# Kernel tuning notes

Measured on AMD Instinct MI355X. Metric: run time of the kernel, lower is better.

Reference implementation:

```python
import jax, jax.numpy as jnp
import numpy as np

N_NODES = 100_000
N_EDGES = 3_200_000
NR = 10_000
NRHO = 10_000
CUTOFF = 6.0
RHO_MAX = 60.0


def natural_cubic_coeffs(x, y):
    """Natural cubic spline coefficients. x:[K], y:[K,C] -> a,b,c,d each [K-1,C]."""
    K, C = y.shape
    h = np.diff(x)
    rhs = 6.0 * ((y[2:] - y[1:-1]) / h[1:, None] - (y[1:-1] - y[:-2]) / h[:-1, None])
    n = K - 2
    diag = 2.0 * (h[:-1] + h[1:])
    off = h[1:-1]
    # Thomas algorithm for the tridiagonal system (natural BC: M[0]=M[K-1]=0)
    cp = np.zeros(n)
    dp = np.zeros((n, C))
    cp[0] = off[0] / diag[0] if n > 1 else 0.0
    dp[0] = rhs[0] / diag[0]
    for i in range(1, n):
        denom = diag[i] - off[i - 1] * cp[i - 1]
        if i < n - 1:
            cp[i] = off[i] / denom
        dp[i] = (rhs[i] - off[i - 1] * dp[i - 1]) / denom
    M = np.zeros((K, C))
    M[n] = dp[n - 1]
    for i in range(n - 2, -1, -1):
        M[i + 1] = dp[i] - cp[i] * M[i + 2]
    a = y[:-1]
    b = (y[1:] - y[:-1]) / h[:, None] - h[:, None] * (2.0 * M[:-1] + M[1:]) / 6.0
    c = M[:-1] / 2.0
    d = (M[1:] - M[:-1]) / (6.0 * h[:, None])
    f32 = lambda z: jnp.asarray(z, dtype=jnp.float32)
    return f32(a), f32(b), f32(c), f32(d)


def spline_eval(x, knots, a, b, c, d):
    """Piecewise cubic eval. x:[M], knots:[K], coeffs:[K-1,C] -> [M,C]."""
    idx = jnp.clip(jnp.searchsorted(knots, x, side='right') - 1, 0, knots.shape[0] - 2)
    s = (x - knots[idx])[:, None]  # offset within segment
    return a[idx] + s * (b[idx] + s * (c[idx] + s * d[idx]))


def setup_inputs() -> dict:
    key = jax.random.key(0)
    k1, k2, k3 = jax.random.split(key, 3)
    # edge displacement vectors; norms ~ chi(3)*1.2, well within cutoff
    r = jax.random.normal(k1, (N_EDGES, 3), dtype=jnp.float32) * 1.2
    src = jax.random.randint(k2, (N_EDGES,), 0, N_NODES, dtype=jnp.int32)
    dst = jax.random.randint(k3, (N_EDGES,), 0, N_NODES, dtype=jnp.int32)
    # synthetic smooth setfl tables (density, r*phi, embedding)
    rs = np.linspace(0.0, CUTOFF, NR)
    rhos_g = np.linspace(0.0, RHO_MAX, NRHO)
    density = np.exp(-rs)
    rphi = 27.2 * 0.529 * np.exp(-2.0 * rs) * (1.0 + 2.0 * rs)
    embedded = -np.sqrt(rhos_g) + 0.05 * rhos_g
    rad_a, rad_b, rad_c, rad_d = natural_cubic_coeffs(rs, np.stack([density, rphi], axis=1))
    emb_a, emb_b, emb_c, emb_d = natural_cubic_coeffs(rhos_g, embedded[:, None])
    return dict(
        r=r, src=src, dst=dst, n_nodes=N_NODES,
        rs=jnp.asarray(rs, jnp.float32), rhos=jnp.asarray(rhos_g, jnp.float32),
        rad_a=rad_a, rad_b=rad_b, rad_c=rad_c, rad_d=rad_d,
        emb_a=emb_a, emb_b=emb_b, emb_c=emb_c, emb_d=emb_d,
    )


def reference(r, src, dst, n_nodes, rs, rhos, rad_a, rad_b, rad_c, rad_d,
              emb_a, emb_b, emb_c, emb_d):
    def energy(r_):
        bl = jnp.linalg.norm(r_, axis=1)                       # [E]
        rp = spline_eval(bl, rs, rad_a, rad_b, rad_c, rad_d)   # [E,2]
        rho_e = rp[:, 0]
        phi_e = rp[:, 1] / bl                                  # rphi / r
        node_rho = jax.ops.segment_sum(rho_e, dst, num_segments=n_nodes)  # [N]
        F = spline_eval(node_rho, rhos, emb_a, emb_b, emb_c, emb_d)[:, 0]
        return jnp.sum(F) + 0.5 * jnp.sum(phi_e)

    E, dEdr = jax.value_and_grad(energy)(r)
    # r_ij = x_dst - x_src  =>  F_k = sum_{src=k} dE/dr - sum_{dst=k} dE/dr
    forces = (jax.ops.segment_sum(dEdr, src, num_segments=n_nodes)
              - jax.ops.segment_sum(dEdr, dst, num_segments=n_nodes))
    return E, forces
```

## Files before the change

kernel.cpp:

```cpp
#include <hip/hip_runtime.h>
#include <math.h>


static constexpr int BLOCK_A = 512;
static constexpr int EPB     = 4096;
static constexpr int SHIFT_P = 12;
static constexpr int NPP     = 4096;
static constexpr int PMAX    = 32;
static constexpr int KR      = 16;
static constexpr int KB      = 24;

static constexpr float QSCALE   = 524288.0f;
static constexpr float QSTEP    = 1.0f / QSCALE;
static constexpr float FSCALE   = 1024.0f;
static constexpr float FSTEP    = 1.0f / FSCALE;

__device__ __forceinline__ double block_reduce_d(double v) {
    #pragma unroll
    for (int off = 32; off > 0; off >>= 1)
        v += __shfl_down(v, off, 64);
    __shared__ double smem[16];
    const int lane = threadIdx.x & 63;
    const int wave = threadIdx.x >> 6;
    if (threadIdx.x < 16) smem[threadIdx.x] = 0.0;
    __syncthreads();
    if (lane == 0) smem[wave] = v;
    __syncthreads();
    if (wave == 0) {
        v = (lane < 16) ? smem[lane] : 0.0;
        #pragma unroll
        for (int off = 8; off > 0; off >>= 1)
            v += __shfl_down(v, off, 64);
    }
    return v;
}

__device__ __forceinline__ int clamp_idx(int i, int hi) {
    return i < 0 ? 0 : (i > hi ? hi : i);
}

__device__ __forceinline__ unsigned f2bf(float f) {
    unsigned u = __float_as_uint(f);
    return (u + 0x7FFFu + ((u >> 16) & 1u)) >> 16;
}
__device__ __forceinline__ float bf2f_hi(unsigned w) {
    return __uint_as_float(w & 0xFFFF0000u);
}
__device__ __forceinline__ float bf2f_lo(unsigned w) {
    return __uint_as_float(w << 16);
}
__device__ __forceinline__ unsigned fq(float f) {
    float s = f * FSCALE;
    s = fminf(fmaxf(s, -1.0e9f), 1.0e9f);
    return (unsigned)(int)rintf(s);
}

__global__ void eam_prep(
    const float* __restrict__ rad_a, const float* __restrict__ rad_b,
    const float* __restrict__ rad_c, const float* __restrict__ rad_d,
    const float* __restrict__ ea, const float* __restrict__ eb,
    const float* __restrict__ ec, const float* __restrict__ ed,
    float4* __restrict__ pack8, float4* __restrict__ pack4,
    int nr1, int nrho1)
{
    const int i = blockIdx.x * 256 + threadIdx.x;
    if (i < nr1) {
        pack8[2*i]   = make_float4(rad_a[2*i], rad_a[2*i+1], rad_b[2*i], rad_b[2*i+1]);
        pack8[2*i+1] = make_float4(rad_c[2*i], rad_c[2*i+1], rad_d[2*i], rad_d[2*i+1]);
    }
    if (i < nrho1)
        pack4[i] = make_float4(ea[i], eb[i], ec[i], ed[i]);
}


__global__ void __launch_bounds__(BLOCK_A) eam_p1a(
    const float* __restrict__ r, const int* __restrict__ dst,
    const float4* __restrict__ pack8,
    unsigned* __restrict__ recR, int* __restrict__ gCurR, double* __restrict__ p1,
    int n_edges, float inv_h, float h, int kmax, int P, int capR)
{
    constexpr int CH = 4 * BLOCK_A;
    __shared__ int hist[PMAX], base[PMAX], cur[PMAX], gbase[PMAX];
    __shared__ int tot;
    __shared__ unsigned buf[CH];
    __shared__ unsigned char pbk[CH];
    const int tid = threadIdx.x;
    const int e0 = blockIdx.x * EPB;
    const int e1 = min(e0 + EPB, n_edges);
    double phi = 0.0;
    for (int c0 = e0; c0 < e1; c0 += CH) {
        int node[4]; float rho[4]; bool val[4];
        if (tid < P) hist[tid] = 0;
        __syncthreads();
        #pragma unroll
        for (int k = 0; k < 4; ++k) {
            const int e = c0 + k * BLOCK_A + tid;
            val[k] = e < e1;
            node[k] = 0; rho[k] = 0.0f;
            if (val[k]) {
                const float x = r[3*e], y = r[3*e+1], z = r[3*e+2];
                const float bl = sqrtf(x*x + y*y + z*z);
                int idx = (int)(bl * inv_h); idx = idx > kmax ? kmax : idx;
                const float s = bl - (float)idx * h;
                const float4 q0 = pack8[2*idx];
                const float4 q1 = pack8[2*idx + 1];
                rho[k] = q0.x + s*(q0.z + s*(q1.x + s*q1.z));
                const float rphi = q0.y + s*(q0.w + s*(q1.y + s*q1.w));
                phi += 0.5 * (double)(rphi / bl);
                node[k] = dst[e];
                atomicAdd(&hist[node[k] >> SHIFT_P], 1);
            }
        }
        __syncthreads();
        if (tid == 0) {
            int s = 0;
            for (int i = 0; i < P; ++i) { base[i] = s; s += hist[i]; }
            tot = s;
        }
        __syncthreads();
        if (tid < P) {
            cur[tid] = base[tid];
            gbase[tid] = hist[tid] ? atomicAdd(&gCurR[tid], hist[tid]) : 0;
        }
        __syncthreads();
        #pragma unroll
        for (int k = 0; k < 4; ++k) {
            if (val[k]) {
                const int pp = node[k] >> SHIFT_P;
                int q = (int)(rho[k] * QSCALE + 0.5f);
                q = q < 0 ? 0 : (q > 0xFFFFF ? 0xFFFFF : q);
                const int pos = atomicAdd(&cur[pp], 1);
                buf[pos] = ((unsigned)(node[k] & (NPP - 1)) << 20) | (unsigned)q;
                pbk[pos] = (unsigned char)pp;
            }
        }
        __syncthreads();
        const int T = tot;
        for (int i = tid; i < T; i += BLOCK_A) {
            const int pp = pbk[i];
            const int gi = gbase[pp] + (i - base[pp]);
            if (gi < capR) recR[(size_t)pp * capR + gi] = buf[i];
        }
        __syncthreads();
    }
    const double bs = block_reduce_d(phi);
    if (tid == 0) p1[blockIdx.x] = bs;
}

__global__ void __launch_bounds__(512) eam_p1b(
    const unsigned* __restrict__ recR, const int* __restrict__ gCurR,
    float* __restrict__ partR, int capR)
{
    __shared__ unsigned acc[NPP];
    const int tid = threadIdx.x;
    const int p = blockIdx.x / KR, j = blockIdx.x % KR;
    for (int i = tid; i < NPP; i += 512) acc[i] = 0u;
    __syncthreads();
    int cnt = gCurR[p]; cnt = cnt > capR ? capR : cnt;
    const int per = (((cnt + KR - 1) / KR) + 3) & ~3;
    const int lo = j * per, hi = min(lo + per, cnt);
    const unsigned* seg = recR + (size_t)p * capR;
    int i = lo + 4 * tid;
    for (; i + 4 * 512 + 3 < hi; i += 2 * 4 * 512) {
        const uint4 a = *(const uint4*)(seg + i);
        const uint4 b = *(const uint4*)(seg + i + 4 * 512);
        atomicAdd(&acc[a.x >> 20], a.x & 0xFFFFFu);
        atomicAdd(&acc[a.y >> 20], a.y & 0xFFFFFu);
        atomicAdd(&acc[a.z >> 20], a.z & 0xFFFFFu);
        atomicAdd(&acc[a.w >> 20], a.w & 0xFFFFFu);
        atomicAdd(&acc[b.x >> 20], b.x & 0xFFFFFu);
        atomicAdd(&acc[b.y >> 20], b.y & 0xFFFFFu);
        atomicAdd(&acc[b.z >> 20], b.z & 0xFFFFFu);
        atomicAdd(&acc[b.w >> 20], b.w & 0xFFFFFu);
    }
    for (; i + 3 < hi; i += 4 * 512) {
        const uint4 a = *(const uint4*)(seg + i);
        atomicAdd(&acc[a.x >> 20], a.x & 0xFFFFFu);
        atomicAdd(&acc[a.y >> 20], a.y & 0xFFFFFu);
        atomicAdd(&acc[a.z >> 20], a.z & 0xFFFFFu);
        atomicAdd(&acc[a.w >> 20], a.w & 0xFFFFFu);
    }
    for (int t = (hi & ~3) + tid; t < hi; t += 512) {
        const unsigned w = seg[t];
        atomicAdd(&acc[w >> 20], w & 0xFFFFFu);
    }
    __syncthreads();
    float* out = partR + (size_t)blockIdx.x * NPP;
    for (int k = tid; k < NPP; k += 512) out[k] = (float)acc[k] * QSTEP;
}

__global__ void __launch_bounds__(1024) eam_p1c(
    const float* __restrict__ partR, const float4* __restrict__ pack4,
    float* __restrict__ Fp, double* __restrict__ p2,
    int n_nodes, float inv_h, float h, int kmax)
{
    const int n = blockIdx.x * 1024 + threadIdx.x;
    double fsum = 0.0;
    if (n < n_nodes) {
        const int p = n >> SHIFT_P, l = n & (NPP - 1);
        float rho = 0.0f;
        #pragma unroll
        for (int j = 0; j < KR; ++j)
            rho += partR[(size_t)(p * KR + j) * NPP + l];
        int idx = clamp_idx((int)(rho * inv_h), kmax);
        const float s = rho - (float)idx * h;
        const float4 q = pack4[idx];
        fsum = (double)(q.x + s*(q.y + s*(q.z + s*q.w)));
        Fp[n] = q.y + s*(2.0f*q.z + 3.0f*q.w*s);
    }
    const double bs = block_reduce_d(fsum);
    if (threadIdx.x == 0) p2[blockIdx.x] = bs;
}


__global__ void __launch_bounds__(BLOCK_A) eam_p3a(
    const float* __restrict__ r, const int* __restrict__ src, const int* __restrict__ dst,
    const float4* __restrict__ pack8, const float* __restrict__ Fp,
    int2* __restrict__ recF, int* __restrict__ gCurF,
    int n_edges, float inv_h, float h, int kmax, int P, int capF)
{
    constexpr int CH = 2 * BLOCK_A;
    __shared__ int hist[PMAX], base[PMAX], cur[PMAX], gbase[PMAX];
    __shared__ int tot;
    __shared__ int2 buf[2 * CH];
    __shared__ unsigned char pbk[2 * CH];
    const int tid = threadIdx.x;
    const int e0 = blockIdx.x * EPB;
    const int e1 = min(e0 + EPB, n_edges);
    for (int c0 = e0; c0 < e1; c0 += CH) {
        int si[2], di[2]; float fx[2], fy[2], fz[2]; bool val[2];
        if (tid < P) hist[tid] = 0;
        __syncthreads();
        #pragma unroll
        for (int k = 0; k < 2; ++k) {
            const int e = c0 + k * BLOCK_A + tid;
            val[k] = e < e1;
            si[k] = 0; di[k] = 0; fx[k] = fy[k] = fz[k] = 0.0f;
            if (val[k]) {
                const float x = r[3*e], y = r[3*e+1], z = r[3*e+2];
                const float bl = sqrtf(x*x + y*y + z*z);
                int idx = (int)(bl * inv_h); idx = idx > kmax ? kmax : idx;
                const float s = bl - (float)idx * h;
                const float4 q0 = pack8[2*idx];
                const float4 q1 = pack8[2*idx + 1];
                const float drho  = q0.z + s*(2.0f*q1.x + 3.0f*q1.z*s);
                const float rphi  = q0.y + s*(q0.w + s*(q1.y + s*q1.w));
                const float drphi = q0.w + s*(2.0f*q1.y + 3.0f*q1.w*s);
                const float inv_bl = 1.0f / bl;
                const float dphi = (drphi - rphi * inv_bl) * inv_bl;
                si[k] = src[e]; di[k] = dst[e];
                const float g = Fp[di[k]] * drho + 0.5f * dphi;
                const float coef = g * inv_bl;
                fx[k] = coef * x; fy[k] = coef * y; fz[k] = coef * z;
                atomicAdd(&hist[si[k] >> SHIFT_P], 1);
                atomicAdd(&hist[di[k] >> SHIFT_P], 1);
            }
        }
        __syncthreads();
        if (tid == 0) {
            int s = 0;
            for (int i = 0; i < P; ++i) { base[i] = s; s += hist[i]; }
            tot = s;
        }
        __syncthreads();
        if (tid < P) {
            cur[tid] = base[tid];
            gbase[tid] = hist[tid] ? atomicAdd(&gCurF[tid], hist[tid]) : 0;
        }
        __syncthreads();
        #pragma unroll
        for (int k = 0; k < 2; ++k) {
            if (val[k]) {
                {
                    const int pp = si[k] >> SHIFT_P;
                    const int pos = atomicAdd(&cur[pp], 1);
                    buf[pos] = make_int2(
                        (int)(((unsigned)(si[k] & (NPP-1)) << 16) | f2bf(fx[k])),
                        (int)((f2bf(fy[k]) << 16) | f2bf(fz[k])));
                    pbk[pos] = (unsigned char)pp;
                }
                {
                    const int pp = di[k] >> SHIFT_P;
                    const int pos = atomicAdd(&cur[pp], 1);
                    buf[pos] = make_int2(
                        (int)(((unsigned)(di[k] & (NPP-1)) << 16) | f2bf(-fx[k])),
                        (int)((f2bf(-fy[k]) << 16) | f2bf(-fz[k])));
                    pbk[pos] = (unsigned char)pp;
                }
            }
        }
        __syncthreads();
        const int T = tot;
        for (int i = tid; i < T; i += BLOCK_A) {
            const int pp = pbk[i];
            const int gi = gbase[pp] + (i - base[pp]);
            if (gi < capF) recF[(size_t)pp * capF + gi] = buf[i];
        }
        __syncthreads();
    }
}

__global__ void __launch_bounds__(512) eam_p3b(
    const int2* __restrict__ recF, const int* __restrict__ gCurF,
    int* __restrict__ partF, int capF)
{
    __shared__ unsigned acc[NPP * 3];
    const int tid = threadIdx.x;
    const int p = blockIdx.x / KB, j = blockIdx.x % KB;
    for (int i = tid; i < NPP * 3; i += 512) acc[i] = 0u;
    __syncthreads();
    int cnt = gCurF[p]; cnt = cnt > capF ? capF : cnt;
    const int per = (((cnt + KB - 1) / KB) + 3) & ~3;
    const int lo = j * per, hi = min(lo + per, cnt);
    const int2* seg = recF + (size_t)p * capF;
    int i = lo + 2 * tid;
    for (; i + 6 * 512 + 1 < hi; i += 8 * 512) {
        const uint4 a = *(const uint4*)(seg + i);
        const uint4 b = *(const uint4*)(seg + i + 2 * 512);
        const uint4 c = *(const uint4*)(seg + i + 4 * 512);
        const uint4 d = *(const uint4*)(seg + i + 6 * 512);
        int li;
        li = (int)(a.x >> 16) * 3;
        atomicAdd(&acc[li+0], fq(bf2f_lo(a.x))); atomicAdd(&acc[li+1], fq(bf2f_hi(a.y))); atomicAdd(&acc[li+2], fq(bf2f_lo(a.y)));
        li = (int)(a.z >> 16) * 3;
        atomicAdd(&acc[li+0], fq(bf2f_lo(a.z))); atomicAdd(&acc[li+1], fq(bf2f_hi(a.w))); atomicAdd(&acc[li+2], fq(bf2f_lo(a.w)));
        li = (int)(b.x >> 16) * 3;
        atomicAdd(&acc[li+0], fq(bf2f_lo(b.x))); atomicAdd(&acc[li+1], fq(bf2f_hi(b.y))); atomicAdd(&acc[li+2], fq(bf2f_lo(b.y)));
        li = (int)(b.z >> 16) * 3;
        atomicAdd(&acc[li+0], fq(bf2f_lo(b.z))); atomicAdd(&acc[li+1], fq(bf2f_hi(b.w))); atomicAdd(&acc[li+2], fq(bf2f_lo(b.w)));
        li = (int)(c.x >> 16) * 3;
        atomicAdd(&acc[li+0], fq(bf2f_lo(c.x))); atomicAdd(&acc[li+1], fq(bf2f_hi(c.y))); atomicAdd(&acc[li+2], fq(bf2f_lo(c.y)));
        li = (int)(c.z >> 16) * 3;
        atomicAdd(&acc[li+0], fq(bf2f_lo(c.z))); atomicAdd(&acc[li+1], fq(bf2f_hi(c.w))); atomicAdd(&acc[li+2], fq(bf2f_lo(c.w)));
        li = (int)(d.x >> 16) * 3;
        atomicAdd(&acc[li+0], fq(bf2f_lo(d.x))); atomicAdd(&acc[li+1], fq(bf2f_hi(d.y))); atomicAdd(&acc[li+2], fq(bf2f_lo(d.y)));
        li = (int)(d.z >> 16) * 3;
        atomicAdd(&acc[li+0], fq(bf2f_lo(d.z))); atomicAdd(&acc[li+1], fq(bf2f_hi(d.w))); atomicAdd(&acc[li+2], fq(bf2f_lo(d.w)));
    }
    for (; i + 1 < hi; i += 2 * 512) {
        const uint4 a = *(const uint4*)(seg + i);
        int li = (int)(a.x >> 16) * 3;
        atomicAdd(&acc[li+0], fq(bf2f_lo(a.x))); atomicAdd(&acc[li+1], fq(bf2f_hi(a.y))); atomicAdd(&acc[li+2], fq(bf2f_lo(a.y)));
        li = (int)(a.z >> 16) * 3;
        atomicAdd(&acc[li+0], fq(bf2f_lo(a.z))); atomicAdd(&acc[li+1], fq(bf2f_hi(a.w))); atomicAdd(&acc[li+2], fq(bf2f_lo(a.w)));
    }
    for (int t = (hi & ~1) + tid; t < hi; t += 512) {
        const int2 rc = seg[t];
        const unsigned w0 = (unsigned)rc.x, w1 = (unsigned)rc.y;
        const int li = (int)(w0 >> 16) * 3;
        atomicAdd(&acc[li+0], fq(bf2f_lo(w0)));
        atomicAdd(&acc[li+1], fq(bf2f_hi(w1)));
        atomicAdd(&acc[li+2], fq(bf2f_lo(w1)));
    }
    __syncthreads();
    int* out = partF + (size_t)blockIdx.x * (NPP * 3);
    for (int k = tid; k < NPP * 3; k += 512) out[k] = (int)acc[k];
}

__global__ void __launch_bounds__(1024) eam_p3c(
    const int* __restrict__ partF, float* __restrict__ outF, int n_nodes)
{
    const int g = blockIdx.x * 1024 + threadIdx.x;
    if (g >= 3 * n_nodes) return;
    const int n = g / 3, c = g - 3 * n;
    const int p = n >> SHIFT_P, l = n & (NPP - 1);
    int v = 0;
    #pragma unroll
    for (int j = 0; j < KB; ++j)
        v += partF[(size_t)(p * KB + j) * (NPP * 3) + l * 3 + c];
    outF[g] = (float)v * FSTEP;
}

__global__ void __launch_bounds__(256) eam_final_e(
    const double* __restrict__ p1, int n1,
    const double* __restrict__ p2, int n2,
    float* __restrict__ outE)
{
    double v = 0.0;
    for (int i = threadIdx.x; i < n1; i += 256) v += p1[i];
    for (int i = threadIdx.x; i < n2; i += 256) v += p2[i];
    const double bs = block_reduce_d(v);
    if (threadIdx.x == 0) *outE = (float)bs;
}


__global__ void __launch_bounds__(256) eam_pass1(
    const float* __restrict__ r, const int* __restrict__ dst,
    const float* __restrict__ rs,
    const float* __restrict__ rad_a, const float* __restrict__ rad_b,
    const float* __restrict__ rad_c, const float* __restrict__ rad_d,
    float* __restrict__ node_rho, double* __restrict__ p1,
    int n_edges, float inv_h, int kmax)
{
    const int e = blockIdx.x * 256 + threadIdx.x;
    double phi_half = 0.0;
    if (e < n_edges) {
        const float x = r[3*e], y = r[3*e+1], z = r[3*e+2];
        const float bl = sqrtf(x*x + y*y + z*z);
        const int idx = clamp_idx((int)(bl * inv_h), kmax);
        const float s = bl - rs[idx];
        const float a0 = rad_a[2*idx], a1 = rad_a[2*idx+1];
        const float b0 = rad_b[2*idx], b1 = rad_b[2*idx+1];
        const float c0 = rad_c[2*idx], c1 = rad_c[2*idx+1];
        const float d0 = rad_d[2*idx], d1 = rad_d[2*idx+1];
        const float rho  = a0 + s*(b0 + s*(c0 + s*d0));
        const float rphi = a1 + s*(b1 + s*(c1 + s*d1));
        unsafeAtomicAdd(&node_rho[dst[e]], rho);
        phi_half = 0.5 * (double)(rphi / bl);
    }
    const double bs = block_reduce_d(phi_half);
    if (threadIdx.x == 0) p1[blockIdx.x] = bs;
}

__global__ void __launch_bounds__(256) eam_pass2(
    const float* __restrict__ node_rho, const float* __restrict__ rhos,
    const float* __restrict__ ea, const float* __restrict__ eb,
    const float* __restrict__ ec, const float* __restrict__ ed,
    float* __restrict__ Fp, double* __restrict__ p2,
    int n_nodes, float inv_h, int kmax)
{
    const int n = blockIdx.x * 256 + threadIdx.x;
    double fsum = 0.0;
    if (n < n_nodes) {
        const float rho = node_rho[n];
        const int idx = clamp_idx((int)(rho * inv_h), kmax);
        const float s = rho - rhos[idx];
        const float A = ea[idx], B = eb[idx], C = ec[idx], D = ed[idx];
        fsum = (double)(A + s*(B + s*(C + s*D)));
        Fp[n] = B + s*(2.0f*C + 3.0f*D*s);
    }
    const double bs = block_reduce_d(fsum);
    if (threadIdx.x == 0) p2[blockIdx.x] = bs;
}

__global__ void __launch_bounds__(256) eam_pass3(
    const float* __restrict__ r, const int* __restrict__ src,
    const int* __restrict__ dst, const float* __restrict__ rs,
    const float* __restrict__ rad_a, const float* __restrict__ rad_b,
    const float* __restrict__ rad_c, const float* __restrict__ rad_d,
    const float* __restrict__ Fp, float* __restrict__ forces,
    int n_edges, float inv_h, int kmax)
{
    const int e = blockIdx.x * 256 + threadIdx.x;
    if (e >= n_edges) return;
    const float x = r[3*e], y = r[3*e+1], z = r[3*e+2];
    const float bl = sqrtf(x*x + y*y + z*z);
    const int idx = clamp_idx((int)(bl * inv_h), kmax);
    const float s = bl - rs[idx];
    const float a1 = rad_a[2*idx+1];
    const float b0 = rad_b[2*idx], b1 = rad_b[2*idx+1];
    const float c0 = rad_c[2*idx], c1 = rad_c[2*idx+1];
    const float d0 = rad_d[2*idx], d1 = rad_d[2*idx+1];
    const float drho  = b0 + s*(2.0f*c0 + 3.0f*d0*s);
    const float rphi  = a1 + s*(b1 + s*(c1 + s*d1));
    const float drphi = b1 + s*(2.0f*c1 + 3.0f*d1*s);
    const float inv_bl = 1.0f / bl;
    const float dphi = (drphi - rphi*inv_bl) * inv_bl;
    const int si = src[e], di = dst[e];
    const float g = Fp[di]*drho + 0.5f*dphi;
    const float coef = g * inv_bl;
    const float fx = coef*x, fy = coef*y, fz = coef*z;
    unsafeAtomicAdd(&forces[3*si+0], fx);
    unsafeAtomicAdd(&forces[3*si+1], fy);
    unsafeAtomicAdd(&forces[3*si+2], fz);
    unsafeAtomicAdd(&forces[3*di+0], -fx);
    unsafeAtomicAdd(&forces[3*di+1], -fy);
    unsafeAtomicAdd(&forces[3*di+2], -fz);
}


extern "C" void kernel_launch(void* const* d_in, const int* in_sizes, int n_in,
                              void* d_out, int out_size, void* d_ws, size_t ws_size,
                              hipStream_t stream) {
    const float* r     = (const float*)d_in[0];
    const int*   src   = (const int*)d_in[1];
    const int*   dst   = (const int*)d_in[2];
    const float* rs    = (const float*)d_in[4];
    const float* rhos  = (const float*)d_in[5];
    const float* rad_a = (const float*)d_in[6];
    const float* rad_b = (const float*)d_in[7];
    const float* rad_c = (const float*)d_in[8];
    const float* rad_d = (const float*)d_in[9];
    const float* ea    = (const float*)d_in[10];
    const float* eb    = (const float*)d_in[11];
    const float* ec    = (const float*)d_in[12];
    const float* ed    = (const float*)d_in[13];

    const int n_edges = in_sizes[0] / 3;
    const int n_nodes = (out_size - 1) / 3;
    const int nr      = in_sizes[4];
    const int nrho    = in_sizes[5];

    float* outE = (float*)d_out;
    float* outF = (float*)d_out + 1;

    const float inv_hr   = (float)((double)(nr - 1) / 6.0);
    const float hr       = (float)(6.0 / (double)(nr - 1));
    const float inv_hrho = (float)((double)(nrho - 1) / 60.0);
    const float hrho     = (float)(60.0 / (double)(nrho - 1));

    auto al = [](size_t x) { return (x + 255) & ~(size_t)255; };
    char* ws = (char*)d_ws;

    const int P    = (n_nodes + NPP - 1) >> SHIFT_P;
    const int nbA  = (n_edges + EPB - 1) / EPB;
    const int nb1c = (n_nodes + 1023) / 1024;
    const int nb3c = (3 * n_nodes + 1023) / 1024;
    const int capR = (n_edges / P + n_edges / (8 * P) + 2048) & ~3;
    const int capF = (2 * n_edges / P + n_edges / (4 * P) + 4096) & ~3;

    size_t off = 0;
    float4*   pack8 = (float4*)(ws + off);   off += al((size_t)(nr - 1) * 32);
    float4*   pack4 = (float4*)(ws + off);   off += al((size_t)(nrho - 1) * 16);
    int*      gCur  = (int*)(ws + off);      off += al((size_t)2 * PMAX * 4);
    float*    Fp    = (float*)(ws + off);    off += al((size_t)n_nodes * 4);
    double*   p1b   = (double*)(ws + off);   off += al((size_t)nbA * 8);
    double*   p2b   = (double*)(ws + off);   off += al((size_t)nb1c * 8);
    float*    partR = (float*)(ws + off);    off += al((size_t)P * KR * NPP * 4);
    int*      partF = (int*)(ws + off);      off += al((size_t)P * KB * NPP * 12);
    unsigned* recR  = (unsigned*)(ws + off); off += al((size_t)P * capR * 4);
    int2*     recF  = (int2*)(ws + off);     off += al((size_t)P * capF * 8);
    const size_t need = off;

    if (P <= PMAX && ws_size >= need) {
        int* gCurR = gCur;
        int* gCurF = gCur + PMAX;
        hipMemsetAsync(gCur, 0, (size_t)2 * PMAX * 4, stream);
        const int npk = (nr - 1) > (nrho - 1) ? (nr - 1) : (nrho - 1);
        eam_prep<<<(npk + 255) / 256, 256, 0, stream>>>(
            rad_a, rad_b, rad_c, rad_d, ea, eb, ec, ed, pack8, pack4, nr - 1, nrho - 1);
        eam_p1a<<<nbA, BLOCK_A, 0, stream>>>(
            r, dst, pack8, recR, gCurR, p1b, n_edges, inv_hr, hr, nr - 2, P, capR);
        eam_p1b<<<P * KR, 512, 0, stream>>>(recR, gCurR, partR, capR);
        eam_p1c<<<nb1c, 1024, 0, stream>>>(
            partR, pack4, Fp, p2b, n_nodes, inv_hrho, hrho, nrho - 2);
        eam_p3a<<<nbA, BLOCK_A, 0, stream>>>(
            r, src, dst, pack8, Fp, recF, gCurF, n_edges, inv_hr, hr, nr - 2, P, capF);
        eam_p3b<<<P * KB, 512, 0, stream>>>(recF, gCurF, partF, capF);
        eam_p3c<<<nb3c, 1024, 0, stream>>>(partF, outF, n_nodes);
        eam_final_e<<<1, 256, 0, stream>>>(p1b, nbA, p2b, nb1c, outE);
    } else {
        size_t o = 0;
        float* node_rho = (float*)(ws + o); o += al((size_t)n_nodes * 4);
        float* Fp2      = (float*)(ws + o); o += al((size_t)n_nodes * 4);
        const int nb_e = (n_edges + 255) / 256;
        const int nb_n = (n_nodes + 255) / 256;
        double* p1 = (double*)(ws + o); o += al((size_t)nb_e * 8);
        double* p2 = (double*)(ws + o);
        hipMemsetAsync(d_out, 0, (size_t)out_size * sizeof(float), stream);
        hipMemsetAsync(node_rho, 0, (size_t)n_nodes * sizeof(float), stream);
        eam_pass1<<<nb_e, 256, 0, stream>>>(r, dst, rs, rad_a, rad_b, rad_c, rad_d,
                                            node_rho, p1, n_edges, inv_hr, nr - 2);
        eam_pass2<<<nb_n, 256, 0, stream>>>(node_rho, rhos, ea, eb, ec, ed,
                                            Fp2, p2, n_nodes, inv_hrho, nrho - 2);
        eam_final_e<<<1, 256, 0, stream>>>(p1, nb_e, p2, nb_n, outE);
        eam_pass3<<<nb_e, 256, 0, stream>>>(r, src, dst, rs, rad_a, rad_b, rad_c, rad_d,
                                            Fp2, outF, n_edges, inv_hr, nr - 2);
    }
}
```

Before: 249.7 us.

## Replace per-chunk histogram/scan binning with fixed-capacity shared slabs and overflow atomics

The edge-binning kernels no longer do a histogram, a serial prefix scan and several block barriers for every chunk. Each block now appends records into a fixed-capacity per-partition slab in shared memory and flushes it once at the end, one wave per partition, with a single global atomic per partition. Records that exceed the slab capacity go to new per-node overflow arrays through global atomics, and those arrays are zeroed with two extra memsets and added back in the reduction kernels. The pass-3 chunk size is also changed, so the number of blocks and the slab sizing move as well. The risk is heavy global-atomic traffic if slabs overflow, plus larger dynamic shared memory per block, which can lower occupancy.

```diff
diff --git a/kernel.cpp b/kernel.cpp
--- a/kernel.cpp
+++ b/kernel.cpp
@@ -2,18 +2,19 @@
 #include <math.h>
 
 
-static constexpr int BLOCK_A = 512;
-static constexpr int EPB     = 4096;
 static constexpr int SHIFT_P = 12;
 static constexpr int NPP     = 4096;
 static constexpr int PMAX    = 32;
 static constexpr int KR      = 16;
 static constexpr int KB      = 24;
-
-static constexpr float QSCALE   = 524288.0f;
-static constexpr float QSTEP    = 1.0f / QSCALE;
-static constexpr float FSCALE   = 1024.0f;
-static constexpr float FSTEP    = 1.0f / FSCALE;
+static constexpr int CH1     = 4096;
+static constexpr int CH3     = 2048;
+static constexpr int CAP     = 256;
+
+static constexpr float QSCALE = 524288.0f;
+static constexpr float QSTEP  = 1.0f / QSCALE;
+static constexpr float FSCALE = 1024.0f;
+static constexpr float FSTEP  = 1.0f / FSCALE;
 
 __device__ __forceinline__ double block_reduce_d(double v) {
     #pragma unroll
@@ -43,12 +44,8 @@
     unsigned u = __float_as_uint(f);
     return (u + 0x7FFFu + ((u >> 16) & 1u)) >> 16;
 }
-__device__ __forceinline__ float bf2f_hi(unsigned w) {
-    return __uint_as_float(w & 0xFFFF0000u);
-}
-__device__ __forceinline__ float bf2f_lo(unsigned w) {
-    return __uint_as_float(w << 16);
-}
+__device__ __forceinline__ float bf2f_hi(unsigned w) { return __uint_as_float(w & 0xFFFF0000u); }
+__device__ __forceinline__ float bf2f_lo(unsigned w) { return __uint_as_float(w << 16); }
 __device__ __forceinline__ unsigned fq(float f) {
     float s = f * FSCALE;
     s = fminf(fmaxf(s, -1.0e9f), 1.0e9f);
@@ -73,78 +70,54 @@
 }
 
 
-__global__ void __launch_bounds__(BLOCK_A) eam_p1a(
+__global__ void __launch_bounds__(512) eam_p1a(
     const float* __restrict__ r, const int* __restrict__ dst,
     const float4* __restrict__ pack8,
-    unsigned* __restrict__ recR, int* __restrict__ gCurR, double* __restrict__ p1,
+    unsigned* __restrict__ recR, int* __restrict__ gCurR,
+    unsigned* __restrict__ ovR, double* __restrict__ p1,
     int n_edges, float inv_h, float h, int kmax, int P, int capR)
 {
-    constexpr int CH = 4 * BLOCK_A;
-    __shared__ int hist[PMAX], base[PMAX], cur[PMAX], gbase[PMAX];
-    __shared__ int tot;
-    __shared__ unsigned buf[CH];
-    __shared__ unsigned char pbk[CH];
-    const int tid = threadIdx.x;
-    const int e0 = blockIdx.x * EPB;
-    const int e1 = min(e0 + EPB, n_edges);
+    extern __shared__ unsigned slabR[];
+    __shared__ int cur[PMAX];
+    const int tid = threadIdx.x, blk = blockIdx.x;
+    for (int b = tid; b < P; b += 512) cur[b] = 0;
+    __syncthreads();
+    const int e0 = blk * CH1, e1 = min(e0 + CH1, n_edges);
     double phi = 0.0;
-    for (int c0 = e0; c0 < e1; c0 += CH) {
-        int node[4]; float rho[4]; bool val[4];
-        if (tid < P) hist[tid] = 0;
-        __syncthreads();
-        #pragma unroll
-        for (int k = 0; k < 4; ++k) {
-            const int e = c0 + k * BLOCK_A + tid;
-            val[k] = e < e1;
-            node[k] = 0; rho[k] = 0.0f;
-            if (val[k]) {
-                const float x = r[3*e], y = r[3*e+1], z = r[3*e+2];
-                const float bl = sqrtf(x*x + y*y + z*z);
-                int idx = (int)(bl * inv_h); idx = idx > kmax ? kmax : idx;
-                const float s = bl - (float)idx * h;
-                const float4 q0 = pack8[2*idx];
-                const float4 q1 = pack8[2*idx + 1];
-                rho[k] = q0.x + s*(q0.z + s*(q1.x + s*q1.z));
-                const float rphi = q0.y + s*(q0.w + s*(q1.y + s*q1.w));
-                phi += 0.5 * (double)(rphi / bl);
-                node[k] = dst[e];
-                atomicAdd(&hist[node[k] >> SHIFT_P], 1);
-            }
+    for (int e = e0 + tid; e < e1; e += 512) {
+        const float x = r[3*e], y = r[3*e+1], z = r[3*e+2];
+        const float bl = sqrtf(x*x + y*y + z*z);
+        int idx = (int)(bl * inv_h); idx = idx > kmax ? kmax : idx;
+        const float s = bl - (float)idx * h;
+        const float4 q0 = pack8[2*idx];
+        const float4 q1 = pack8[2*idx + 1];
+        const float rho  = q0.x + s*(q0.z + s*(q1.x + s*q1.z));
+        const float rphi = q0.y + s*(q0.w + s*(q1.y + s*q1.w));
+        phi += 0.5 * (double)(rphi / bl);
+        const int node = dst[e];
+        const int pp = node >> SHIFT_P;
+        int q = (int)(rho * QSCALE + 0.5f);
+        q = q < 0 ? 0 : (q > 0xFFFFF ? 0xFFFFF : q);
+        const int slot = atomicAdd(&cur[pp], 1);
+        if (slot < CAP)
+            slabR[pp * CAP + slot] = ((unsigned)(node & (NPP - 1)) << 20) | (unsigned)q;
+        else
+            atomicAdd(&ovR[node], (unsigned)q);
+    }
+    __syncthreads();
+    const int wave = tid >> 6, lane = tid & 63;
+    for (int p = wave; p < P; p += 8) {
+        int c = cur[p]; c = c > CAP ? CAP : c;
+        int gb = 0;
+        if (lane == 0 && c > 0) gb = atomicAdd(&gCurR[p], c);
+        gb = __shfl(gb, 0, 64);
+        for (int i = lane; i < c; i += 64) {
+            const int gi = gb + i;
+            if (gi < capR) recR[(size_t)p * capR + gi] = slabR[p * CAP + i];
         }
-        __syncthreads();
-        if (tid == 0) {
-            int s = 0;
-            for (int i = 0; i < P; ++i) { base[i] = s; s += hist[i]; }
-            tot = s;
-        }
-        __syncthreads();
-        if (tid < P) {
-            cur[tid] = base[tid];
-            gbase[tid] = hist[tid] ? atomicAdd(&gCurR[tid], hist[tid]) : 0;
-        }
-        __syncthreads();
-        #pragma unroll
-        for (int k = 0; k < 4; ++k) {
-            if (val[k]) {
-                const int pp = node[k] >> SHIFT_P;
-                int q = (int)(rho[k] * QSCALE + 0.5f);
-                q = q < 0 ? 0 : (q > 0xFFFFF ? 0xFFFFF : q);
-                const int pos = atomicAdd(&cur[pp], 1);
-                buf[pos] = ((unsigned)(node[k] & (NPP - 1)) << 20) | (unsigned)q;
-                pbk[pos] = (unsigned char)pp;
-            }
-        }
-        __syncthreads();
-        const int T = tot;
-        for (int i = tid; i < T; i += BLOCK_A) {
-            const int pp = pbk[i];
-            const int gi = gbase[pp] + (i - base[pp]);
-            if (gi < capR) recR[(size_t)pp * capR + gi] = buf[i];
-        }
-        __syncthreads();
     }
     const double bs = block_reduce_d(phi);
-    if (tid == 0) p1[blockIdx.x] = bs;
+    if (tid == 0) p1[blk] = bs;
 }
 
 __global__ void __launch_bounds__(512) eam_p1b(
@@ -190,7 +163,8 @@
 }
 
 __global__ void __launch_bounds__(1024) eam_p1c(
-    const float* __restrict__ partR, const float4* __restrict__ pack4,
+    const float* __restrict__ partR, const unsigned* __restrict__ ovR,
+    const float4* __restrict__ pack4,
     float* __restrict__ Fp, double* __restrict__ p2,
     int n_nodes, float inv_h, float h, int kmax)
 {
@@ -198,7 +172,7 @@
     double fsum = 0.0;
     if (n < n_nodes) {
         const int p = n >> SHIFT_P, l = n & (NPP - 1);
-        float rho = 0.0f;
+        float rho = (float)(int)ovR[n] * QSTEP;
         #pragma unroll
         for (int j = 0; j < KR; ++j)
             rho += partR[(size_t)(p * KR + j) * NPP + l];
@@ -213,90 +187,73 @@
 }
 
 
-__global__ void __launch_bounds__(BLOCK_A) eam_p3a(
+__global__ void __launch_bounds__(512) eam_p3a(
     const float* __restrict__ r, const int* __restrict__ src, const int* __restrict__ dst,
     const float4* __restrict__ pack8, const float* __restrict__ Fp,
     int2* __restrict__ recF, int* __restrict__ gCurF,
+    unsigned* __restrict__ ovF,
     int n_edges, float inv_h, float h, int kmax, int P, int capF)
 {
-    constexpr int CH = 2 * BLOCK_A;
-    __shared__ int hist[PMAX], base[PMAX], cur[PMAX], gbase[PMAX];
-    __shared__ int tot;
-    __shared__ int2 buf[2 * CH];
-    __shared__ unsigned char pbk[2 * CH];
-    const int tid = threadIdx.x;
-    const int e0 = blockIdx.x * EPB;
-    const int e1 = min(e0 + EPB, n_edges);
-    for (int c0 = e0; c0 < e1; c0 += CH) {
-        int si[2], di[2]; float fx[2], fy[2], fz[2]; bool val[2];
-        if (tid < P) hist[tid] = 0;
-        __syncthreads();
-        #pragma unroll
-        for (int k = 0; k < 2; ++k) {
-            const int e = c0 + k * BLOCK_A + tid;
-            val[k] = e < e1;
-            si[k] = 0; di[k] = 0; fx[k] = fy[k] = fz[k] = 0.0f;
-            if (val[k]) {
-                const float x = r[3*e], y = r[3*e+1], z = r[3*e+2];
-                const float bl = sqrtf(x*x + y*y + z*z);
-                int idx = (int)(bl * inv_h); idx = idx > kmax ? kmax : idx;
-                const float s = bl - (float)idx * h;
-                const float4 q0 = pack8[2*idx];
-                const float4 q1 = pack8[2*idx + 1];
-                const float drho  = q0.z + s*(2.0f*q1.x + 3.0f*q1.z*s);
-                const float rphi  = q0.y + s*(q0.w + s*(q1.y + s*q1.w));
-                const float drphi = q0.w + s*(2.0f*q1.y + 3.0f*q1.w*s);
-                const float inv_bl = 1.0f / bl;
-                const float dphi = (drphi - rphi * inv_bl) * inv_bl;
-                si[k] = src[e]; di[k] = dst[e];
-                const float g = Fp[di[k]] * drho + 0.5f * dphi;
-                const float coef = g * inv_bl;
-                fx[k] = coef * x; fy[k] = coef * y; fz[k] = coef * z;
-                atomicAdd(&hist[si[k] >> SHIFT_P], 1);
-                atomicAdd(&hist[di[k] >> SHIFT_P], 1);
+    extern __shared__ int2 slabF[];
+    __shared__ int cur[PMAX];
+    const int tid = threadIdx.x, blk = blockIdx.x;
+    for (int b = tid; b < P; b += 512) cur[b] = 0;
+    __syncthreads();
+    const int e0 = blk * CH3, e1 = min(e0 + CH3, n_edges);
+    for (int e = e0 + tid; e < e1; e += 512) {
+        const float x = r[3*e], y = r[3*e+1], z = r[3*e+2];
+        const float bl = sqrtf(x*x + y*y + z*z);
+        int idx = (int)(bl * inv_h); idx = idx > kmax ? kmax : idx;
+        const float s = bl - (float)idx * h;
+        const float4 q0 = pack8[2*idx];
+        const float4 q1 = pack8[2*idx + 1];
+        const float drho  = q0.z + s*(2.0f*q1.x + 3.0f*q1.z*s);
+        const float rphi  = q0.y + s*(q0.w + s*(q1.y + s*q1.w));
+        const float drphi = q0.w + s*(2.0f*q1.y + 3.0f*q1.w*s);
+        const float inv_bl = 1.0f / bl;
+        const float dphi = (drphi - rphi * inv_bl) * inv_bl;
+        const int si = src[e], di = dst[e];
+        const float g = Fp[di] * drho + 0.5f * dphi;
+        const float coef = g * inv_bl;
+        const float fx = coef * x, fy = coef * y, fz = coef * z;
+        {
+            const int pp = si >> SHIFT_P;
+            const int slot = atomicAdd(&cur[pp], 1);
+            if (slot < CAP)
+                slabF[pp * CAP + slot] = make_int2(
+                    (int)(((unsigned)(si & (NPP-1)) << 16) | f2bf(fx)),
+                    (int)((f2bf(fy) << 16) | f2bf(fz)));
+            else {
+                atomicAdd(&ovF[3*si+0], fq(fx));
+                atomicAdd(&ovF[3*si+1], fq(fy));
+                atomicAdd(&ovF[3*si+2], fq(fz));
             }
         }
-        __syncthreads();
-        if (tid == 0) {
-            int s = 0;
-            for (int i = 0; i < P; ++i) { base[i] = s; s += hist[i]; }
-            tot = s;
-        }
-        __syncthreads();
-        if (tid < P) {
-            cur[tid] = base[tid];
-            gbase[tid] = hist[tid] ? atomicAdd(&gCurF[tid], hist[tid]) : 0;
-        }
-        __syncthreads();
-        #pragma unroll
-        for (int k = 0; k < 2; ++k) {
-            if (val[k]) {
-                {
-                    const int pp = si[k] >> SHIFT_P;
-                    const int pos = atomicAdd(&cur[pp], 1);
-                    buf[pos] = make_int2(
-                        (int)(((unsigned)(si[k] & (NPP-1)) << 16) | f2bf(fx[k])),
-                        (int)((f2bf(fy[k]) << 16) | f2bf(fz[k])));
-                    pbk[pos] = (unsigned char)pp;
-                }
-                {
-                    const int pp = di[k] >> SHIFT_P;
-                    const int pos = atomicAdd(&cur[pp], 1);
-                    buf[pos] = make_int2(
-                        (int)(((unsigned)(di[k] & (NPP-1)) << 16) | f2bf(-fx[k])),
-                        (int)((f2bf(-fy[k]) << 16) | f2bf(-fz[k])));
-                    pbk[pos] = (unsigned char)pp;
-                }
+        {
+            const int pp = di >> SHIFT_P;
+            const int slot = atomicAdd(&cur[pp], 1);
+            if (slot < CAP)
+                slabF[pp * CAP + slot] = make_int2(
+                    (int)(((unsigned)(di & (NPP-1)) << 16) | f2bf(-fx)),
+                    (int)((f2bf(-fy) << 16) | f2bf(-fz)));
+            else {
+                atomicAdd(&ovF[3*di+0], fq(-fx));
+                atomicAdd(&ovF[3*di+1], fq(-fy));
+                atomicAdd(&ovF[3*di+2], fq(-fz));
             }
         }
-        __syncthreads();
-        const int T = tot;
-        for (int i = tid; i < T; i += BLOCK_A) {
-            const int pp = pbk[i];
-            const int gi = gbase[pp] + (i - base[pp]);
-            if (gi < capF) recF[(size_t)pp * capF + gi] = buf[i];
+    }
+    __syncthreads();
+    const int wave = tid >> 6, lane = tid & 63;
+    for (int p = wave; p < P; p += 8) {
+        int c = cur[p]; c = c > CAP ? CAP : c;
+        int gb = 0;
+        if (lane == 0 && c > 0) gb = atomicAdd(&gCurF[p], c);
+        gb = __shfl(gb, 0, 64);
+        for (int i = lane; i < c; i += 64) {
+            const int gi = gb + i;
+            if (gi < capF) recF[(size_t)p * capF + gi] = slabF[p * CAP + i];
         }
-        __syncthreads();
     }
 }
 
@@ -358,13 +315,14 @@
 }
 
 __global__ void __launch_bounds__(1024) eam_p3c(
-    const int* __restrict__ partF, float* __restrict__ outF, int n_nodes)
+    const int* __restrict__ partF, const unsigned* __restrict__ ovF,
+    float* __restrict__ outF, int n_nodes)
 {
     const int g = blockIdx.x * 1024 + threadIdx.x;
     if (g >= 3 * n_nodes) return;
     const int n = g / 3, c = g - 3 * n;
     const int p = n >> SHIFT_P, l = n & (NPP - 1);
-    int v = 0;
+    int v = (int)ovF[g];
     #pragma unroll
     for (int j = 0; j < KB; ++j)
         v += partF[(size_t)(p * KB + j) * (NPP * 3) + l * 3 + c];
@@ -503,7 +461,8 @@
     char* ws = (char*)d_ws;
 
     const int P    = (n_nodes + NPP - 1) >> SHIFT_P;
-    const int nbA  = (n_edges + EPB - 1) / EPB;
+    const int nb1a = (n_edges + CH1 - 1) / CH1;
+    const int nb3a = (n_edges + CH3 - 1) / CH3;
     const int nb1c = (n_nodes + 1023) / 1024;
     const int nb3c = (3 * n_nodes + 1023) / 1024;
     const int capR = (n_edges / P + n_edges / (8 * P) + 2048) & ~3;
@@ -513,8 +472,10 @@
     float4*   pack8 = (float4*)(ws + off);   off += al((size_t)(nr - 1) * 32);
     float4*   pack4 = (float4*)(ws + off);   off += al((size_t)(nrho - 1) * 16);
     int*      gCur  = (int*)(ws + off);      off += al((size_t)2 * PMAX * 4);
+    unsigned* ovR   = (unsigned*)(ws + off); off += al((size_t)n_nodes * 4);
+    unsigned* ovF   = (unsigned*)(ws + off); off += al((size_t)n_nodes * 12);
     float*    Fp    = (float*)(ws + off);    off += al((size_t)n_nodes * 4);
-    double*   p1b   = (double*)(ws + off);   off += al((size_t)nbA * 8);
+    double*   p1b   = (double*)(ws + off);   off += al((size_t)nb1a * 8);
     double*   p2b   = (double*)(ws + off);   off += al((size_t)nb1c * 8);
     float*    partR = (float*)(ws + off);    off += al((size_t)P * KR * NPP * 4);
     int*      partF = (int*)(ws + off);      off += al((size_t)P * KB * NPP * 12);
@@ -526,19 +487,21 @@
         int* gCurR = gCur;
         int* gCurF = gCur + PMAX;
         hipMemsetAsync(gCur, 0, (size_t)2 * PMAX * 4, stream);
+        hipMemsetAsync(ovR, 0, (size_t)n_nodes * 4, stream);
+        hipMemsetAsync(ovF, 0, (size_t)n_nodes * 12, stream);
         const int npk = (nr - 1) > (nrho - 1) ? (nr - 1) : (nrho - 1);
         eam_prep<<<(npk + 255) / 256, 256, 0, stream>>>(
             rad_a, rad_b, rad_c, rad_d, ea, eb, ec, ed, pack8, pack4, nr - 1, nrho - 1);
-        eam_p1a<<<nbA, BLOCK_A, 0, stream>>>(
-            r, dst, pack8, recR, gCurR, p1b, n_edges, inv_hr, hr, nr - 2, P, capR);
+        eam_p1a<<<nb1a, 512, (size_t)P * CAP * 4, stream>>>(
+            r, dst, pack8, recR, gCurR, ovR, p1b, n_edges, inv_hr, hr, nr - 2, P, capR);
         eam_p1b<<<P * KR, 512, 0, stream>>>(recR, gCurR, partR, capR);
         eam_p1c<<<nb1c, 1024, 0, stream>>>(
-            partR, pack4, Fp, p2b, n_nodes, inv_hrho, hrho, nrho - 2);
-        eam_p3a<<<nbA, BLOCK_A, 0, stream>>>(
-            r, src, dst, pack8, Fp, recF, gCurF, n_edges, inv_hr, hr, nr - 2, P, capF);
+            partR, ovR, pack4, Fp, p2b, n_nodes, inv_hrho, hrho, nrho - 2);
+        eam_p3a<<<nb3a, 512, (size_t)P * CAP * 8, stream>>>(
+            r, src, dst, pack8, Fp, recF, gCurF, ovF, n_edges, inv_hr, hr, nr - 2, P, capF);
         eam_p3b<<<P * KB, 512, 0, stream>>>(recF, gCurF, partF, capF);
-        eam_p3c<<<nb3c, 1024, 0, stream>>>(partF, outF, n_nodes);
-        eam_final_e<<<1, 256, 0, stream>>>(p1b, nbA, p2b, nb1c, outE);
+        eam_p3c<<<nb3c, 1024, 0, stream>>>(partF, ovF, outF, n_nodes);
+        eam_final_e<<<1, 256, 0, stream>>>(p1b, nb1a, p2b, nb1c, outE);
     } else {
         size_t o = 0;
         float* node_rho = (float*)(ws + o); o += al((size_t)n_nodes * 4);
```

Measured after the change: 633.9 us. 2.54x slower.
